# Optimization experiments

Hardware: AMD Instinct MI355X
Metric: run time of the kernel (lower is better)

The kernel has to match this reference:

```python
import math
import jax, jax.numpy as jnp
import numpy as np

ABS_MAX = 1000000.0
SCALE = 0.1   # kernel_params['scale']
C = 1.0       # kernel_params['c'] (additive constant, order=2 polynomial)
IN_DIM = 16
OUT_DIM = 64
N_NODES = 50000
N_EDGES = 400000
EXP_DIM = 1 + IN_DIM + IN_DIM * IN_DIM  # 273


def poly2_expand(x):
    """Exact feature map of (z.z' + c)^2 with z = SCALE*x.
    phi(z) = [c, sqrt(2c)*z, vec(z z^T)] -> dim 1 + d + d^2."""
    z = SCALE * x                                   # [N, d]
    const = jnp.full(z.shape[:-1] + (1,), C, dtype=z.dtype)
    lin = math.sqrt(2.0 * C) * z                    # [N, d]
    quad = (z[:, :, None] * z[:, None, :]).reshape(z.shape[0], -1)  # [N, d^2]
    return jnp.concatenate([const, lin, quad], axis=-1)


def setup_inputs() -> dict:
    key = jax.random.key(0)
    k1, k2, k3, k4 = jax.random.split(key, 4)
    features = jax.random.normal(k1, (N_NODES, IN_DIM), dtype=jnp.float32)
    src = jax.random.randint(k2, (N_EDGES,), 0, N_NODES, dtype=jnp.int32)
    dst = jax.random.randint(k3, (N_EDGES,), 0, N_NODES, dtype=jnp.int32)
    proj = jax.random.normal(k4, (EXP_DIM, OUT_DIM), dtype=jnp.float32)
    proj = proj / jnp.linalg.norm(proj, axis=0, keepdims=True)  # random unit vectors
    return {"features": features, "src": src, "dst": dst, "proj": proj}


def reference(features, src, dst, proj):
    # RKHS lifting + clamp
    h = jnp.clip(poly2_expand(features), -ABS_MAX, ABS_MAX)   # [N, EXP_DIM]
    # copy_src + sum aggregation over edges (scatter-add at dst)
    agg = jax.ops.segment_sum(h[src], dst, num_segments=N_NODES)
    agg = jnp.clip(agg, -ABS_MAX, ABS_MAX)
    # cat_scale == 0 branch: residual add of expanded features
    feat = jnp.clip(agg + h, -ABS_MAX, ABS_MAX)
    # random projection reduction, scaled by 1/sqrt(in_dim)
    out = (feat @ proj) / math.sqrt(IN_DIM)                   # [N, OUT_DIM]
    return out
```

## Files before the change

### kernel.cpp

```cpp
#include <hip/hip_runtime.h>

#define IN_DIM   16
#define OUT_DIM  64
#define N_NODES  50000
#define N_EDGES  400000
#define SCALE    0.1f
#define SQRT2C   1.41421356237309515f
#define KPAD     288
#define DEG_PAD  48

#define NODE_UNITS 782
#define HIST_UNITS 391

typedef _Float16 f16x8 __attribute__((ext_vector_type(8)));
typedef float    f32x4 __attribute__((ext_vector_type(4)));

__global__ __launch_bounds__(256) void setup_kernel(
    const float* __restrict__ proj, int* __restrict__ cnt,
    _Float16* __restrict__ B16)
{
    const int t = blockIdx.x * 256 + threadIdx.x;
    if (t < N_NODES) cnt[t] = 0;
    if (t < OUT_DIM * 512) {
        const int col = t >> 9;
        const int k   = t & 511;
        if (k < KPAD) {
            float pv;
            if      (k < 256)  pv = proj[(17 + k) * OUT_DIM + col];
            else if (k == 256) pv = proj[0 * OUT_DIM + col];
            else if (k < 273)  pv = proj[(k - 256) * OUT_DIM + col];
            else               pv = 0.0f;
            B16[col * KPAD + k] = (_Float16)pv;
        }
    }
}

__device__ __forceinline__ void node_unit(
    int blk, const float* __restrict__ features,
    const _Float16* __restrict__ B16, _Float16* __restrict__ y16)
{
    const int tid  = threadIdx.x;
    const int wave = tid >> 6;
    const int lane = tid & 63;
    const int kg   = lane >> 4;
    const int bcol = lane & 15;

    const int m0 = blk * 64 + wave * 16;

    float z[IN_DIM];
    {
        int n = m0 + (lane & 15); if (n >= N_NODES) n = N_NODES - 1;
        const float4* f4 = (const float4*)(features + n * IN_DIM);
        #pragma unroll
        for (int q = 0; q < 4; ++q) {
            float4 v = f4[q];
            z[q*4+0] = SCALE * v.x; z[q*4+1] = SCALE * v.y;
            z[q*4+2] = SCALE * v.z; z[q*4+3] = SCALE * v.w;
        }
    }

    f32x4 acc[4] = {};

    #pragma unroll
    for (int kk = 0; kk < 9; ++kk) {
        f16x8 a;
        if (kk < 8) {
            const float zi = z[kk * 2 + (kg >> 1)];
            const int jb = (kg & 1) * 8;
            #pragma unroll
            for (int j = 0; j < 8; ++j) a[j] = (_Float16)(zi * z[jb + j]);
        } else {
            if (kg == 0) {
                a[0] = (_Float16)1.0f;
                #pragma unroll
                for (int j = 1; j < 8; ++j) a[j] = (_Float16)(SQRT2C * z[j - 1]);
            } else if (kg == 1) {
                #pragma unroll
                for (int j = 0; j < 8; ++j) a[j] = (_Float16)(SQRT2C * z[7 + j]);
            } else if (kg == 2) {
                a[0] = (_Float16)(SQRT2C * z[15]);
                #pragma unroll
                for (int j = 1; j < 8; ++j) a[j] = (_Float16)0.0f;
            } else {
                #pragma unroll
                for (int j = 0; j < 8; ++j) a[j] = (_Float16)0.0f;
            }
        }

        #pragma unroll
        for (int nt = 0; nt < 4; ++nt) {
            const f16x8 b = *(const f16x8*)&B16[(nt * 16 + bcol) * KPAD + kk * 32 + kg * 8];
            acc[nt] = __builtin_amdgcn_mfma_f32_16x16x32_f16(a, b, acc[nt], 0, 0, 0);
        }
    }

    #pragma unroll
    for (int nt = 0; nt < 4; ++nt) {
        #pragma unroll
        for (int r = 0; r < 4; ++r) {
            const int c = nt * 16 + bcol;
            const int n = m0 + kg * 4 + r;
            if (n < N_NODES) y16[n * OUT_DIM + c] = (_Float16)acc[nt][r];
        }
    }
}

__device__ __forceinline__ void hist_unit4(
    int blk, const int* __restrict__ src, const int* __restrict__ dst,
    int* __restrict__ cnt, unsigned short* __restrict__ eidx)
{
    const int base = blk * 1024 + threadIdx.x;
    #pragma unroll
    for (int k = 0; k < 4; ++k) {
        const int e = base + k * 256;
        if (e < N_EDGES) {
            const int d = dst[e];
            const int p = atomicAdd(&cnt[d], 1);
            if (p < DEG_PAD) eidx[d * DEG_PAD + p] = (unsigned short)src[e];
        }
    }
}

__global__ __launch_bounds__(256) void fused_node_hist(
    const float* __restrict__ features, const _Float16* __restrict__ B16,
    _Float16* __restrict__ y16,
    const int* __restrict__ src, const int* __restrict__ dst,
    int* __restrict__ cnt, unsigned short* __restrict__ eidx)
{
    if (blockIdx.x < NODE_UNITS)
        node_unit(blockIdx.x, features, B16, y16);
    else
        hist_unit4(blockIdx.x - NODE_UNITS, src, dst, cnt, eidx);
}

__global__ __launch_bounds__(256) void pull_kernel(
    const int* __restrict__ cnt, const unsigned short* __restrict__ eidx,
    const _Float16* __restrict__ y16, float* __restrict__ out)
{
    const int wave = threadIdx.x >> 6;
    const int lane = threadIdx.x & 63;
    const int n    = blockIdx.x * 4 + wave;
    if (n >= N_NODES) return;

    const int g = lane >> 3;
    const int q = lane & 7;

    int deg = cnt[n];
    if (deg > DEG_PAD) deg = DEG_PAD;

    int myIdx = 0;
    if (lane < DEG_PAD) myIdx = eidx[n * DEG_PAD + lane];

    float a0=0.f,a1=0.f,a2=0.f,a3=0.f,a4=0.f,a5=0.f,a6=0.f,a7=0.f;
    if (g == 0) {
        const f16x8 r = *(const f16x8*)(y16 + (size_t)n * OUT_DIM + q * 8);
        a0=(float)r[0]; a1=(float)r[1]; a2=(float)r[2]; a3=(float)r[3];
        a4=(float)r[4]; a5=(float)r[5]; a6=(float)r[6]; a7=(float)r[7];
    }

    for (int k = 0; k < deg; k += 8) {
        const int e = k + g;
        const int s = __shfl(myIdx, e, 64);
        const f16x8 v = *(const f16x8*)(y16 + (size_t)s * OUT_DIM + q * 8);
        if (e < deg) {
            a0+=(float)v[0]; a1+=(float)v[1]; a2+=(float)v[2]; a3+=(float)v[3];
            a4+=(float)v[4]; a5+=(float)v[5]; a6+=(float)v[6]; a7+=(float)v[7];
        }
    }

    #pragma unroll
    for (int off = 8; off <= 32; off <<= 1) {
        a0 += __shfl_xor(a0, off, 64); a1 += __shfl_xor(a1, off, 64);
        a2 += __shfl_xor(a2, off, 64); a3 += __shfl_xor(a3, off, 64);
        a4 += __shfl_xor(a4, off, 64); a5 += __shfl_xor(a5, off, 64);
        a6 += __shfl_xor(a6, off, 64); a7 += __shfl_xor(a7, off, 64);
    }

    if (g == 0) {
        float* o = out + (size_t)n * OUT_DIM + q * 8;
        float4 lo, hi;
        lo.x = 0.25f*a0; lo.y = 0.25f*a1; lo.z = 0.25f*a2; lo.w = 0.25f*a3;
        hi.x = 0.25f*a4; hi.y = 0.25f*a5; hi.z = 0.25f*a6; hi.w = 0.25f*a7;
        *(float4*)o       = lo;
        *(float4*)(o + 4) = hi;
    }
}

extern "C" void kernel_launch(void* const* d_in, const int* in_sizes, int n_in,
                              void* d_out, int out_size, void* d_ws, size_t ws_size,
                              hipStream_t stream)
{
    const float* features = (const float*)d_in[0];
    const int*   src      = (const int*)  d_in[1];
    const int*   dst      = (const int*)  d_in[2];
    const float* proj     = (const float*)d_in[3];

    float* out = (float*)d_out;

    _Float16*       y16  = (_Float16*)d_ws;
    int*            cnt  = (int*)((char*)d_ws + (size_t)N_NODES * OUT_DIM * 2);
    unsigned short* eidx = (unsigned short*)((char*)cnt + (size_t)N_NODES * 4);
    _Float16*       B16  = (_Float16*)((char*)eidx + (size_t)N_NODES * DEG_PAD * 2);

    const int setupBlocks = (N_NODES + 255) / 256;
    setup_kernel<<<setupBlocks, 256, 0, stream>>>(proj, cnt, B16);

    fused_node_hist<<<NODE_UNITS + HIST_UNITS, 256, 0, stream>>>(
        features, B16, y16, src, dst, cnt, eidx);

    const int pullBlocks = (N_NODES + 3) / 4;
    pull_kernel<<<pullBlocks, 256, 0, stream>>>(cnt, eidx, y16, out);
}
```

Baseline: 54.63 us.

## Map one node per 8-lane group in pull kernel with batched neighbor loads

The pull kernel now gives each 8-lane group its own node, so one wave handles 8 nodes instead of 1. The cross-group shuffle reduction and the idle lanes for low-degree nodes go away. Neighbor indices are read in chunks of 8 and their rows gathered in an unrolled loop, which puts up to 8 independent loads in flight per lane. The trade-off is redundant index loads across the 8 lanes of a group and divergence when nodes in the same wave have different degrees. Nodes with degree at most 8 always issue 8 gathers, which may read padding slots.

```diff
diff --git a/kernel.cpp b/kernel.cpp
--- a/kernel.cpp
+++ b/kernel.cpp
@@ -139,51 +139,58 @@
 {
     const int wave = threadIdx.x >> 6;
     const int lane = threadIdx.x & 63;
-    const int n    = blockIdx.x * 4 + wave;
+    const int grp  = lane >> 3;
+    const int lq   = lane & 7;
+    const int n    = blockIdx.x * 32 + wave * 8 + grp;
     if (n >= N_NODES) return;
-
-    const int g = lane >> 3;
-    const int q = lane & 7;
 
     int deg = cnt[n];
     if (deg > DEG_PAD) deg = DEG_PAD;
 
-    int myIdx = 0;
-    if (lane < DEG_PAD) myIdx = eidx[n * DEG_PAD + lane];
-
-    float a0=0.f,a1=0.f,a2=0.f,a3=0.f,a4=0.f,a5=0.f,a6=0.f,a7=0.f;
-    if (g == 0) {
-        const f16x8 r = *(const f16x8*)(y16 + (size_t)n * OUT_DIM + q * 8);
+    const unsigned short* slots = eidx + (size_t)n * DEG_PAD;
+
+    float a0,a1,a2,a3,a4,a5,a6,a7;
+    {
+        const f16x8 r = *(const f16x8*)(y16 + (size_t)n * OUT_DIM + lq * 8);
         a0=(float)r[0]; a1=(float)r[1]; a2=(float)r[2]; a3=(float)r[3];
         a4=(float)r[4]; a5=(float)r[5]; a6=(float)r[6]; a7=(float)r[7];
     }
 
-    for (int k = 0; k < deg; k += 8) {
-        const int e = k + g;
-        const int s = __shfl(myIdx, e, 64);
-        const f16x8 v = *(const f16x8*)(y16 + (size_t)s * OUT_DIM + q * 8);
-        if (e < deg) {
-            a0+=(float)v[0]; a1+=(float)v[1]; a2+=(float)v[2]; a3+=(float)v[3];
-            a4+=(float)v[4]; a5+=(float)v[5]; a6+=(float)v[6]; a7+=(float)v[7];
-        }
-    }
-
-    #pragma unroll
-    for (int off = 8; off <= 32; off <<= 1) {
-        a0 += __shfl_xor(a0, off, 64); a1 += __shfl_xor(a1, off, 64);
-        a2 += __shfl_xor(a2, off, 64); a3 += __shfl_xor(a3, off, 64);
-        a4 += __shfl_xor(a4, off, 64); a5 += __shfl_xor(a5, off, 64);
-        a6 += __shfl_xor(a6, off, 64); a7 += __shfl_xor(a7, off, 64);
-    }
-
-    if (g == 0) {
-        float* o = out + (size_t)n * OUT_DIM + q * 8;
-        float4 lo, hi;
-        lo.x = 0.25f*a0; lo.y = 0.25f*a1; lo.z = 0.25f*a2; lo.w = 0.25f*a3;
-        hi.x = 0.25f*a4; hi.y = 0.25f*a5; hi.z = 0.25f*a6; hi.w = 0.25f*a7;
-        *(float4*)o       = lo;
-        *(float4*)(o + 4) = hi;
-    }
+    {
+        int idx[8];
+        #pragma unroll
+        for (int j = 0; j < 8; ++j) idx[j] = slots[j];
+        #pragma unroll
+        for (int j = 0; j < 8; ++j) {
+            const f16x8 v = *(const f16x8*)(y16 + (size_t)idx[j] * OUT_DIM + lq * 8);
+            if (j < deg) {
+                a0+=(float)v[0]; a1+=(float)v[1]; a2+=(float)v[2]; a3+=(float)v[3];
+                a4+=(float)v[4]; a5+=(float)v[5]; a6+=(float)v[6]; a7+=(float)v[7];
+            }
+        }
+    }
+
+    for (int k0 = 8; k0 < DEG_PAD; k0 += 8) {
+        if (k0 >= deg) break;
+        int idx[8];
+        #pragma unroll
+        for (int j = 0; j < 8; ++j) idx[j] = slots[k0 + j];
+        #pragma unroll
+        for (int j = 0; j < 8; ++j) {
+            const f16x8 v = *(const f16x8*)(y16 + (size_t)idx[j] * OUT_DIM + lq * 8);
+            if (k0 + j < deg) {
+                a0+=(float)v[0]; a1+=(float)v[1]; a2+=(float)v[2]; a3+=(float)v[3];
+                a4+=(float)v[4]; a5+=(float)v[5]; a6+=(float)v[6]; a7+=(float)v[7];
+            }
+        }
+    }
+
+    float* o = out + (size_t)n * OUT_DIM + lq * 8;
+    float4 lo, hi;
+    lo.x = 0.25f*a0; lo.y = 0.25f*a1; lo.z = 0.25f*a2; lo.w = 0.25f*a3;
+    hi.x = 0.25f*a4; hi.y = 0.25f*a5; hi.z = 0.25f*a6; hi.w = 0.25f*a7;
+    *(float4*)o       = lo;
+    *(float4*)(o + 4) = hi;
 }
 
 extern "C" void kernel_launch(void* const* d_in, const int* in_sizes, int n_in,
@@ -208,6 +215,6 @@
     fused_node_hist<<<NODE_UNITS + HIST_UNITS, 256, 0, stream>>>(
         features, B16, y16, src, dst, cnt, eidx);
 
-    const int pullBlocks = (N_NODES + 3) / 4;
+    const int pullBlocks = (N_NODES + 31) / 32;
     pull_kernel<<<pullBlocks, 256, 0, stream>>>(cnt, eidx, y16, out);
 }
```

After: 48.52 us. 1.13x faster.
